# Kernel optimization log

Measured on AMD Instinct MI355X. Metric: run time of the kernel, lower is better.

Reference implementation:

```python
import jax, jax.numpy as jnp
import numpy as np

B, N, F, H = 2, 256, 64, 4
HID = 64            # hidden_features
C = H * HID         # n_coefficients = 256
KF = 50             # kernel_features (rbf count)
CUTOFF_UPPER = 5.0  # ExpNormalSmearing default (lower = 0)
ALPHA = 5.0 / CUTOFF_UPPER


def _dense(key, din, dout):
    scale = 1.0 / np.sqrt(din)
    return jax.random.uniform(key, (din, dout), minval=-scale, maxval=scale).astype(jnp.float32)


def setup_inputs() -> dict:
    key = jax.random.key(0)
    ks = jax.random.split(key, 16)
    start = float(np.exp(-CUTOFF_UPPER))
    means = jnp.asarray(np.linspace(start, 1.0, KF), jnp.float32)
    betas = jnp.full((KF,), (2.0 / KF * (1.0 - start)) ** -2, dtype=jnp.float32)
    d_edge_in = 2 * F              # h_cat_ht width
    d_cat = 2 * F + KF + 1         # concat([h0, rbf*h, dist])
    return dict(
        h=jax.random.normal(ks[0], (B, N, F), jnp.float32),
        x=jax.random.normal(ks[1], (B, N, 3), jnp.float32),
        v=jax.random.normal(ks[2], (B, N, 3), jnp.float32) * 0.1,
        W_in=_dense(ks[3], d_edge_in, KF), b_in=jnp.zeros((KF,), jnp.float32),
        rbf_means=means, rbf_betas=betas,
        W_o1=_dense(ks[4], d_cat, HID), b_o1=jnp.zeros((HID,), jnp.float32),
        W_o2=_dense(ks[5], HID, HID), b_o2=jnp.zeros((HID,), jnp.float32),
        W_sem=_dense(ks[6], HID, H), b_sem=jnp.zeros((H,), jnp.float32),
        W_xmix=_dense(ks[7], C, C),
        W_p1=_dense(ks[8], C, HID), b_p1=jnp.zeros((HID,), jnp.float32),
        W_p2=_dense(ks[9], HID, HID), b_p2=jnp.zeros((HID,), jnp.float32),
        W_n1=_dense(ks[10], F + C + HID, HID), b_n1=jnp.zeros((HID,), jnp.float32),
        W_n2=_dense(ks[11], HID, F), b_n2=jnp.zeros((F,), jnp.float32),
        W_v1=_dense(ks[12], F, HID), b_v1=jnp.zeros((HID,), jnp.float32),
        W_v2=_dense(ks[13], HID, 1),
        W_vmix=_dense(ks[14], C, 1),
    )


def reference(h, x, v, W_in, b_in, rbf_means, rbf_betas, W_o1, b_o1, W_o2, b_o2,
              W_sem, b_sem, W_xmix, W_p1, b_p1, W_p2, b_p2,
              W_n1, b_n1, W_n2, b_n2, W_v1, b_v1, W_v2, W_vmix):
    silu = jax.nn.silu
    n = h.shape[-2]
    # all-pairs displacements: entry [i, j] = x_j - x_i  (get_x_minus_xt)
    x_minus_xt = x[..., None, :, :] - x[..., :, None, :]                       # [B,N,N,3]
    d = jnp.sqrt(jax.nn.relu((x_minus_xt ** 2).sum(-1, keepdims=True)) + 1e-5)  # [B,N,N,1]
    # h_cat_ht: concat([h_j, h_i]) per pair (get_h_cat_ht)
    h_j = jnp.broadcast_to(h[..., None, :, :], h.shape[:-2] + (n, n, h.shape[-1]))
    h_i = jnp.broadcast_to(h[..., :, None, :], h.shape[:-2] + (n, n, h.shape[-1]))
    h_cat = jnp.concatenate([h_j, h_i], -1)                                     # [B,N,N,2F]
    # --- edge model: ContinuousFilterConvolutionWithConcatenation ---
    h1 = h_cat @ W_in + b_in                                                    # [B,N,N,KF]
    cut = 0.5 * (jnp.cos(d * jnp.pi / CUTOFF_UPPER) + 1.0) * (d < CUTOFF_UPPER)
    rbf = cut * jnp.exp(-rbf_betas * (jnp.exp(-ALPHA * d) - rbf_means) ** 2)    # [B,N,N,KF]
    h_e_mtx = silu(jnp.concatenate([h_cat, rbf * h1, d], -1) @ W_o1 + b_o1) @ W_o2 + b_o2  # [B,N,N,HID]
    # --- semantic attention (cutoff=None => euclidean factor is 1.0) ---
    att = jax.nn.celu(h_e_mtx @ W_sem + b_sem, alpha=2.0)                       # [B,N,N,H]
    att = att - 1e5 * jnp.eye(n, dtype=att.dtype)[..., None]                    # mask self-pairs
    att = jax.nn.softmax(att, axis=-2)
    combined = att / att.sum(-2, keepdims=True)                                 # combined_attention
    # per-head weighted edge features, flattened (feature-major, head-minor)
    h_e_att = (h_e_mtx[..., :, None] * combined[..., None, :]).reshape(h_e_mtx.shape[:-1] + (C,))  # [B,N,N,C]
    # --- spatial attention ---
    coeff = jnp.tanh(h_e_att @ W_xmix)                                          # x_mixing, [B,N,N,C]
    x_hat = x_minus_xt / (d + 1e-5)                                             # [B,N,N,3]
    # combinations[b,i,j,c,:] = x_hat[b,i,j,:] * coeff[b,i,j,c]; mean over j, fused:
    comb_sum = jnp.einsum('bijc,bijd->bicd', coeff, x_hat) / n                  # [B,N,C,3]
    comb_norm = (comb_sum ** 2).sum(-1)                                         # [B,N,C]
    h_comb = silu(silu(comb_norm @ W_p1 + b_p1) @ W_p2 + b_p2)                  # post_norm_mlp
    # --- aggregate + node model (residual) ---
    h_e = h_e_att.sum(-2)                                                       # [B,N,C]
    h_new = h + silu(silu(jnp.concatenate([h, h_e, h_comb], -1) @ W_n1 + b_n1) @ W_n2 + b_n2)
    # --- velocity / coordinate update (v_mixing then mean over j, fused via comb_sum) ---
    delta_v = jnp.einsum('bicd,c->bid', comb_sum, W_vmix[:, 0])                 # [B,N,3]
    v_scale = 2.0 * jax.nn.sigmoid(silu(h_new @ W_v1 + b_v1) @ W_v2)            # velocity_mlp + double_sigmoid
    v_new = delta_v + v_scale * v
    x_new = x + v_new
    return (h_new, x_new, v_new)
```

## Files before the change

### kernel.cpp

```cpp
#include <hip/hip_runtime.h>
#include <hip/hip_bf16.h>

typedef __hip_bfloat16 bf16;
typedef __attribute__((ext_vector_type(8))) short bf16x8;
typedef __attribute__((ext_vector_type(4))) float f32x4;

#define NNODE 512

__device__ __forceinline__ float b2f(bf16 v){ return __bfloat162float(v); }
__device__ __forceinline__ float siluf(float x){ return x / (1.f + __expf(-x)); }
__device__ __forceinline__ float tanhfast(float x){ return 1.f - 2.f/(__expf(2.f*x)+1.f); }
__device__ __forceinline__ float celu2(float x){ return x > 0.f ? x : 2.f*(__expf(0.5f*x)-1.f); }
__device__ __forceinline__ float bs2f(short v){ union{unsigned int i; float f;} t; t.i = ((unsigned int)(unsigned short)v) << 16; return t.f; }
__device__ __forceinline__ short f2bs(float x){ union{ bf16 b; short s; } u; u.b = __float2bfloat16(x); return u.s; }
__device__ __forceinline__ float lo16f(unsigned int u){ union{unsigned int i; float f;} t; t.i = u<<16; return t.f; }
__device__ __forceinline__ float hi16f(unsigned int u){ union{unsigned int i; float f;} t; t.i = u & 0xffff0000u; return t.f; }

template<typename T> __device__ __forceinline__ float ldv(const void* p, int i);
template<> __device__ __forceinline__ float ldv<float>(const void* p, int i){ return ((const float*)p)[i]; }
template<> __device__ __forceinline__ float ldv<bf16 >(const void* p, int i){ return b2f(((const bf16*)p)[i]); }

template<typename T> __device__ __forceinline__ void stv(void* p, int i, float v);
template<> __device__ __forceinline__ void stv<float>(void* p, int i, float v){ ((float*)p)[i] = v; }
template<> __device__ __forceinline__ void stv<bf16 >(void* p, int i, float v){ ((bf16*)p)[i] = __float2bfloat16(v); }

template<typename T> __device__ __forceinline__ short ldbs(const void* p, int i);
template<> __device__ __forceinline__ short ldbs<bf16 >(const void* p, int i){ union{ bf16 b; short s; } u; u.b = ((const bf16*)p)[i]; return u.s; }
template<> __device__ __forceinline__ short ldbs<float>(const void* p, int i){ return f2bs(((const float*)p)[i]); }

struct Args {
    const void *h,*x,*v,*Win,*bin,*means,*betas,*Wo1,*bo1,*Wo2,*bo2,*Wsem,*bsem,*Wx,
               *Wp1,*bp1,*Wp2,*bp2,*Wn1,*bn1,*Wn2,*bn2,*Wv1,*bv1,*Wv2,*Wvm;
};

__global__ void k_detect(const void* means, int* flag){
    if (threadIdx.x == 0){
        float v = b2f(((const bf16*)means)[0]);
        flag[0] = (fabsf(v) > 1.0f || v != v) ? 1 : 0;
    }
}

template<typename T>
__device__ __forceinline__ void nodepre_body(const Args& A, short* __restrict__ U1,
                                             float* __restrict__ Aj, short* __restrict__ WxT,
                                             float* sh)
{
    int bn = blockIdx.x, t = threadIdx.x;
    sh[t] = ldv<T>(A.h, bn*64 + t);
    __syncthreads();
    float u1 = 0.f;
    for (int f = 0; f < 64; ++f) u1 += sh[f] * ldv<T>(A.Wo1, f*64 + t);
    U1[bn*64 + t] = f2bs(u1);
    if (t < 50){
        float a1 = 0.f;
        for (int f = 0; f < 64; ++f) a1 += sh[f] * ldv<T>(A.Win, f*50 + t);
        Aj[bn*64 + t] = a1;
    }
    int o = (bn*64 + t)*2;
    #pragma unroll
    for (int q = 0; q < 2; ++q){
        int oo = o + q;
        int hh = oo >> 14, rem = oo & 16383, n = rem >> 6, f = rem & 63;
        WxT[oo] = ldbs<T>(A.Wx, (4*f + hh)*256 + n);
    }
}

__global__ void __launch_bounds__(64) k_nodepre(Args A, const int* __restrict__ flag,
                                                short* __restrict__ U1, float* __restrict__ Aj,
                                                short* __restrict__ WxT)
{
    __shared__ float sh[64];
    if (flag[0]) nodepre_body<float>(A, U1, Aj, WxT, sh);
    else         nodepre_body<bf16 >(A, U1, Aj, WxT, sh);
}

struct SmemPost {
    __align__(16) float att[256][4];
    float part[2][256];
    float red[768];
    float cn[256];
    float he[256];
    float fa[64];
    float fb[64];
    float mpart[8][64];
    float tmp[8][4];
};
struct SmemEdge {
    __align__(16) short wo1t[64*72];
    __align__(16) short wo2t[64*72];
};
struct Smem {
    __align__(16) bf16  e[256][72];
    __align__(16) float x4[256][4];
    float hi[64];
    float u2[64];
    float bo1v[64];
    float wl[64];
    float aivs[64];
    short wsem[256];
    __align__(16) short rbfh[8][4][72];
    __align__(16) short mid[8][4][72];
    union { SmemEdge edge; SmemPost post; } u;
};

template<typename T>
__device__ __forceinline__ void sake_body(const Args& A,
        const short* __restrict__ U1w, const float* __restrict__ Ajw,
        const short* __restrict__ wxt, void* __restrict__ out, Smem& S)
{
    int bi = blockIdx.x;
    int b = bi >> 8, i = bi & 255;
    int tid = threadIdx.x, w = tid >> 6, lane = tid & 63;
    int lane15 = lane & 15, quad = lane >> 4;

    if (tid < 64)  S.hi[tid]   = ldv<T>(A.h, bi*64 + tid);
    if (tid < 256) S.wsem[tid] = ldbs<T>(A.Wsem, tid);
    #pragma unroll
    for (int q = 0; q < 8; ++q){
        int idx = q*512 + tid;
        int n = idx >> 6, k = idx & 63;
        S.u.edge.wo2t[n*72 + k] = ldbs<T>(A.Wo2, k*64 + n);
        S.u.edge.wo1t[n*72 + k] = (k < 50) ? ldbs<T>(A.Wo1, (128+k)*64 + n) : (short)0;
    }
    if (lane >= 50){
        #pragma unroll
        for (int pp = 0; pp < 4; ++pp) S.rbfh[w][pp][lane] = 0;
    }
    float xi0 = ldv<T>(A.x, bi*3+0), xi1 = ldv<T>(A.x, bi*3+1), xi2 = ldv<T>(A.x, bi*3+2);
    if (tid < 256){
        int j = tid;
        float dx = ldv<T>(A.x,(b*256+j)*3+0) - xi0;
        float dy = ldv<T>(A.x,(b*256+j)*3+1) - xi1;
        float dz = ldv<T>(A.x,(b*256+j)*3+2) - xi2;
        float dd = sqrtf(dx*dx + dy*dy + dz*dz + 1e-5f);
        float inv = 1.f/(dd + 1e-5f);
        S.x4[j][0] = dx*inv; S.x4[j][1] = dy*inv; S.x4[j][2] = dz*inv; S.x4[j][3] = dd;
    }
    __syncthreads();

    if (w == 0){
        float u2v = 0.f;
        for (int f = 0; f < 64; ++f) u2v += S.hi[f] * ldv<T>(A.Wo1, (64+f)*64 + lane);
        S.u2[lane]   = u2v;
        S.bo1v[lane] = ldv<T>(A.bo1, lane);
        S.wl[lane]   = ldv<T>(A.Wo1, 178*64 + lane);
    } else if (w == 1 && lane < 50){
        float av = 0.f;
        for (int f = 0; f < 64; ++f) av += S.hi[f] * ldv<T>(A.Win, (64+f)*50 + lane);
        S.aivs[lane] = av;
    }
    float muv = 0.f, bev = 0.f, binv = 0.f;
    if (lane < 50){
        muv = ldv<T>(A.means, lane); bev = ldv<T>(A.betas, lane); binv = ldv<T>(A.bin, lane);
    }
    __syncthreads();

    float aiv = (lane < 50) ? S.aivs[lane] : 0.f;
    float bo2c[4], u24[4], bo14[4], wl4[4];
    #pragma unroll
    for (int nf = 0; nf < 4; ++nf){
        bo2c[nf] = ldv<T>(A.bo2, nf*16 + lane15);
        u24[nf]  = S.u2[nf*16 + lane15];
        bo14[nf] = S.bo1v[nf*16 + lane15];
        wl4[nf]  = S.wl[nf*16 + lane15];
    }

    for (int pass = 0; pass < 8; ++pass){
        int j0 = pass*32 + w*4;
        float dist[4];
        #pragma unroll
        for (int pp = 0; pp < 4; ++pp) dist[pp] = S.x4[j0+pp][3];

        if (lane < 50){
            #pragma unroll
            for (int pp = 0; pp < 4; ++pp){
                int j = j0 + pp;
                float h1 = Ajw[(b*256+j)*64 + lane] + aiv + binv;
                float dd = dist[pp];
                float cut = (dd < 5.f) ? 0.5f*(__cosf(dd*0.6283185307f) + 1.f) : 0.f;
                float ex = __expf(-dd) - muv;
                S.rbfh[w][pp][lane] = f2bs(cut * __expf(-bev*ex*ex) * h1);
            }
        }

        bf16x8 ar[2];
        #pragma unroll
        for (int kk = 0; kk < 2; ++kk){
            bf16x8 av = (bf16x8){0,0,0,0,0,0,0,0};
            if (lane15 < 4) av = *(const bf16x8*)&S.rbfh[w][lane15][kk*32 + quad*8];
            ar[kk] = av;
        }
        #pragma unroll
        for (int nf = 0; nf < 4; ++nf){
            int n = nf*16 + lane15;
            f32x4 Co1 = (f32x4){0.f,0.f,0.f,0.f};
            if (quad == 0){
                #pragma unroll
                for (int r = 0; r < 4; ++r)
                    Co1[r] = bs2f(U1w[(b*256 + j0 + r)*64 + n]) + u24[nf] + bo14[nf] + dist[r]*wl4[nf];
            }
            bf16x8 b0 = *(const bf16x8*)&S.u.edge.wo1t[n*72 + quad*8];
            bf16x8 b1 = *(const bf16x8*)&S.u.edge.wo1t[n*72 + 32 + quad*8];
            Co1 = __builtin_amdgcn_mfma_f32_16x16x32_bf16(ar[0], b0, Co1, 0, 0, 0);
            Co1 = __builtin_amdgcn_mfma_f32_16x16x32_bf16(ar[1], b1, Co1, 0, 0, 0);
            if (quad == 0){
                #pragma unroll
                for (int r = 0; r < 4; ++r) S.mid[w][r][n] = f2bs(siluf(Co1[r]));
            }
        }

        bf16x8 av2[2];
        #pragma unroll
        for (int kk = 0; kk < 2; ++kk){
            bf16x8 av = (bf16x8){0,0,0,0,0,0,0,0};
            if (lane15 < 4) av = *(const bf16x8*)&S.mid[w][lane15][kk*32 + quad*8];
            av2[kk] = av;
        }
        #pragma unroll
        for (int nf = 0; nf < 4; ++nf){
            int n = nf*16 + lane15;
            f32x4 Cc2 = (f32x4){bo2c[nf], bo2c[nf], bo2c[nf], bo2c[nf]};
            bf16x8 b0 = *(const bf16x8*)&S.u.edge.wo2t[n*72 + quad*8];
            bf16x8 b1 = *(const bf16x8*)&S.u.edge.wo2t[n*72 + 32 + quad*8];
            Cc2 = __builtin_amdgcn_mfma_f32_16x16x32_bf16(av2[0], b0, Cc2, 0, 0, 0);
            Cc2 = __builtin_amdgcn_mfma_f32_16x16x32_bf16(av2[1], b1, Cc2, 0, 0, 0);
            if (quad == 0){
                S.e[j0+0][n] = __float2bfloat16(Cc2[0]);
                S.e[j0+1][n] = __float2bfloat16(Cc2[1]);
                S.e[j0+2][n] = __float2bfloat16(Cc2[2]);
                S.e[j0+3][n] = __float2bfloat16(Cc2[3]);
            }
        }
    }
    __syncthreads();

    float ex0 = 0.f, ex1 = 0.f, ex2 = 0.f, ex3 = 0.f;
    if (tid < 256){
        int j = tid;
        float a0 = ldv<T>(A.bsem,0), a1 = ldv<T>(A.bsem,1), a2 = ldv<T>(A.bsem,2), a3 = ldv<T>(A.bsem,3);
        const unsigned int* erow = (const unsigned int*)&S.e[j][0];
        for (int f2 = 0; f2 < 32; ++f2){
            unsigned int u0 = erow[f2];
            float e0 = lo16f(u0), e1 = hi16f(u0);
            a0 += e0*bs2f(S.wsem[f2*8+0]) + e1*bs2f(S.wsem[f2*8+4]);
            a1 += e0*bs2f(S.wsem[f2*8+1]) + e1*bs2f(S.wsem[f2*8+5]);
            a2 += e0*bs2f(S.wsem[f2*8+2]) + e1*bs2f(S.wsem[f2*8+6]);
            a3 += e0*bs2f(S.wsem[f2*8+3]) + e1*bs2f(S.wsem[f2*8+7]);
        }
        a0 = celu2(a0); a1 = celu2(a1); a2 = celu2(a2); a3 = celu2(a3);
        if (j == i){ a0 -= 1e5f; a1 -= 1e5f; a2 -= 1e5f; a3 -= 1e5f; }
        float m0 = a0, m1 = a1, m2 = a2, m3 = a3;
        #pragma unroll
        for (int off = 1; off < 64; off <<= 1){
            m0 = fmaxf(m0, __shfl_xor(m0, off)); m1 = fmaxf(m1, __shfl_xor(m1, off));
            m2 = fmaxf(m2, __shfl_xor(m2, off)); m3 = fmaxf(m3, __shfl_xor(m3, off));
        }
        if (lane == 0){
            S.u.post.tmp[w][0] = m0; S.u.post.tmp[w][1] = m1;
            S.u.post.tmp[w][2] = m2; S.u.post.tmp[w][3] = m3;
        }
        ex0 = a0; ex1 = a1; ex2 = a2; ex3 = a3;
    }
    __syncthreads();
    if (tid < 256){
        float m0 = fmaxf(fmaxf(S.u.post.tmp[0][0], S.u.post.tmp[1][0]), fmaxf(S.u.post.tmp[2][0], S.u.post.tmp[3][0]));
        float m1 = fmaxf(fmaxf(S.u.post.tmp[0][1], S.u.post.tmp[1][1]), fmaxf(S.u.post.tmp[2][1], S.u.post.tmp[3][1]));
        float m2 = fmaxf(fmaxf(S.u.post.tmp[0][2], S.u.post.tmp[1][2]), fmaxf(S.u.post.tmp[2][2], S.u.post.tmp[3][2]));
        float m3 = fmaxf(fmaxf(S.u.post.tmp[0][3], S.u.post.tmp[1][3]), fmaxf(S.u.post.tmp[2][3], S.u.post.tmp[3][3]));
        ex0 = __expf(ex0-m0); ex1 = __expf(ex1-m1); ex2 = __expf(ex2-m2); ex3 = __expf(ex3-m3);
        float s0 = ex0, s1 = ex1, s2 = ex2, s3 = ex3;
        #pragma unroll
        for (int off = 1; off < 64; off <<= 1){
            s0 += __shfl_xor(s0, off); s1 += __shfl_xor(s1, off);
            s2 += __shfl_xor(s2, off); s3 += __shfl_xor(s3, off);
        }
        if (lane == 0){
            S.u.post.tmp[4+w][0] = s0; S.u.post.tmp[4+w][1] = s1;
            S.u.post.tmp[4+w][2] = s2; S.u.post.tmp[4+w][3] = s3;
        }
    }
    __syncthreads();
    if (tid < 256){
        float s0 = S.u.post.tmp[4][0]+S.u.post.tmp[5][0]+S.u.post.tmp[6][0]+S.u.post.tmp[7][0];
        float s1 = S.u.post.tmp[4][1]+S.u.post.tmp[5][1]+S.u.post.tmp[6][1]+S.u.post.tmp[7][1];
        float s2 = S.u.post.tmp[4][2]+S.u.post.tmp[5][2]+S.u.post.tmp[6][2]+S.u.post.tmp[7][2];
        float s3 = S.u.post.tmp[4][3]+S.u.post.tmp[5][3]+S.u.post.tmp[6][3]+S.u.post.tmp[7][3];
        S.u.post.att[tid][0] = ex0/s0; S.u.post.att[tid][1] = ex1/s1;
        S.u.post.att[tid][2] = ex2/s2; S.u.post.att[tid][3] = ex3/s3;
    }
    __syncthreads();

    {
        int c = tid & 255, jh = tid >> 8;
        int f_he = c >> 2, h_he = c & 3;
        float acc = 0.f;
        int j2 = jh*128;
        for (int q = 0; q < 128; ++q, ++j2)
            acc += b2f(S.e[j2][f_he]) * S.u.post.att[j2][h_he];
        S.u.post.part[jh][c] = acc;
    }
    __syncthreads();
    if (tid < 256) S.u.post.he[tid] = S.u.post.part[0][tid] + S.u.post.part[1][tid];

    {
        const short* se_s = (const short*)S.e;
        float ca[2][3];
        #pragma unroll
        for (int nf2 = 0; nf2 < 2; ++nf2){ ca[nf2][0]=0.f; ca[nf2][1]=0.f; ca[nf2][2]=0.f; }

        #pragma unroll
        for (int nf2 = 0; nf2 < 2; ++nf2){
            int n = w*32 + nf2*16 + lane15;
            bf16x8 Bh[4][2];
            #pragma unroll
            for (int hh = 0; hh < 4; ++hh){
                const short* bp = wxt + (hh*256 + n)*64 + quad*8;
                Bh[hh][0] = *(const bf16x8*)(bp);
                Bh[hh][1] = *(const bf16x8*)(bp + 32);
            }
            for (int mt = 0; mt < 16; ++mt){
                int jq = mt*16 + quad*4;
                f32x4 att4[4];
                #pragma unroll
                for (int r = 0; r < 4; ++r) att4[r] = *(const f32x4*)&S.u.post.att[jq + r][0];
                bf16x8 Af[2];
                #pragma unroll
                for (int ks = 0; ks < 2; ++ks)
                    Af[ks] = *(const bf16x8*)(se_s + (mt*16 + lane15)*72 + ks*32 + quad*8);
                float Pt[4] = {0.f, 0.f, 0.f, 0.f};
                #pragma unroll
                for (int hh = 0; hh < 4; ++hh){
                    f32x4 Cc = (f32x4){0.f,0.f,0.f,0.f};
                    Cc = __builtin_amdgcn_mfma_f32_16x16x32_bf16(Af[0], Bh[hh][0], Cc, 0, 0, 0);
                    Cc = __builtin_amdgcn_mfma_f32_16x16x32_bf16(Af[1], Bh[hh][1], Cc, 0, 0, 0);
                    #pragma unroll
                    for (int r = 0; r < 4; ++r) Pt[r] += att4[r][hh] * Cc[r];
                }
                #pragma unroll
                for (int r = 0; r < 4; ++r){
                    int j = jq + r;
                    float cf = tanhfast(Pt[r]);
                    f32x4 xh = *(const f32x4*)&S.x4[j][0];
                    ca[nf2][0] += cf*xh[0]; ca[nf2][1] += cf*xh[1]; ca[nf2][2] += cf*xh[2];
                }
            }
        }
        #pragma unroll
        for (int nf2 = 0; nf2 < 2; ++nf2){
            #pragma unroll
            for (int d = 0; d < 3; ++d){
                float vs = ca[nf2][d];
                vs += __shfl_xor(vs, 16);
                vs += __shfl_xor(vs, 32);
                if (quad == 0) S.u.post.red[(w*32 + nf2*16 + lane15)*3 + d] = vs;
            }
        }
    }
    __syncthreads();

    const float sc = 1.f/256.f;
    if (tid < 256){
        float c0 = S.u.post.red[tid*3+0]*sc, c1 = S.u.post.red[tid*3+1]*sc, c2 = S.u.post.red[tid*3+2]*sc;
        S.u.post.cn[tid] = c0*c0 + c1*c1 + c2*c2;
    }
    __syncthreads();

    {
        float acc = 0.f;
        int c0 = w*32;
        for (int c = c0; c < c0+32; ++c) acc += S.u.post.cn[c] * ldv<T>(A.Wp1, c*64 + lane);
        S.u.post.mpart[w][lane] = acc;
    }
    __syncthreads();
    if (tid < 64){
        float acc = ldv<T>(A.bp1, tid);
        #pragma unroll
        for (int q = 0; q < 8; ++q) acc += S.u.post.mpart[q][tid];
        S.u.post.fa[tid] = siluf(acc);
    }
    __syncthreads();
    {
        float acc = 0.f;
        int k0 = w*8;
        #pragma unroll
        for (int k = 0; k < 8; ++k) acc += S.u.post.fa[k0+k] * ldv<T>(A.Wp2, (k0+k)*64 + lane);
        S.u.post.mpart[w][lane] = acc;
    }
    __syncthreads();
    if (tid < 64){
        float acc = ldv<T>(A.bp2, tid);
        #pragma unroll
        for (int q = 0; q < 8; ++q) acc += S.u.post.mpart[q][tid];
        S.u.post.fb[tid] = siluf(acc);
    }
    __syncthreads();
    {
        float acc = 0.f;
        int r0 = w*48;
        for (int r = r0; r < r0+48; ++r){
            float xv = (r < 64) ? S.hi[r] : (r < 320) ? S.u.post.he[r-64] : S.u.post.fb[r-320];
            acc += xv * ldv<T>(A.Wn1, r*64 + lane);
        }
        S.u.post.mpart[w][lane] = acc;
    }
    __syncthreads();
    if (tid < 64){
        float acc = ldv<T>(A.bn1, tid);
        #pragma unroll
        for (int q = 0; q < 8; ++q) acc += S.u.post.mpart[q][tid];
        S.u.post.fa[tid] = siluf(acc);
    }
    __syncthreads();
    {
        float acc = 0.f;
        int k0 = w*8;
        #pragma unroll
        for (int k = 0; k < 8; ++k) acc += S.u.post.fa[k0+k] * ldv<T>(A.Wn2, (k0+k)*64 + lane);
        S.u.post.mpart[w][lane] = acc;
    }
    __syncthreads();
    if (tid < 64){
        float acc = ldv<T>(A.bn2, tid);
        #pragma unroll
        for (int q = 0; q < 8; ++q) acc += S.u.post.mpart[q][tid];
        float hn = S.hi[tid] + siluf(acc);
        stv<T>(out, bi*64 + tid, hn);
        S.u.post.fb[tid] = hn;
    }
    __syncthreads();
    {
        float acc = 0.f;
        int k0 = w*8;
        #pragma unroll
        for (int k = 0; k < 8; ++k) acc += S.u.post.fb[k0+k] * ldv<T>(A.Wv1, (k0+k)*64 + lane);
        S.u.post.mpart[w][lane] = acc;
    }
    __syncthreads();
    float vscale = 0.f;
    if (tid < 64){
        float acc = ldv<T>(A.bv1, tid);
        #pragma unroll
        for (int q = 0; q < 8; ++q) acc += S.u.post.mpart[q][tid];
        float term = siluf(acc) * ldv<T>(A.Wv2, tid);
        #pragma unroll
        for (int off = 1; off < 64; off <<= 1) term += __shfl_xor(term, off);
        vscale = 2.f / (1.f + __expf(-term));
    }
    if (w < 4){
        int c = w*64 + lane;
        float wv = ldv<T>(A.Wvm, c);
        float d0 = S.u.post.red[c*3+0]*sc*wv;
        float d1 = S.u.post.red[c*3+1]*sc*wv;
        float d2 = S.u.post.red[c*3+2]*sc*wv;
        #pragma unroll
        for (int off = 1; off < 64; off <<= 1){
            d0 += __shfl_xor(d0, off); d1 += __shfl_xor(d1, off); d2 += __shfl_xor(d2, off);
        }
        if (lane == 0){ S.u.post.tmp[w][0] = d0; S.u.post.tmp[w][1] = d1; S.u.post.tmp[w][2] = d2; }
    }
    __syncthreads();
    if (tid < 3){
        float dv = S.u.post.tmp[0][tid] + S.u.post.tmp[1][tid] + S.u.post.tmp[2][tid] + S.u.post.tmp[3][tid];
        float vn = dv + vscale * ldv<T>(A.v, bi*3 + tid);
        float xn = ldv<T>(A.x, bi*3 + tid) + vn;
        stv<T>(out, 32768 + bi*3 + tid, xn);
        stv<T>(out, 34304 + bi*3 + tid, vn);
    }
}

__global__ void __launch_bounds__(512, 4) k_sake(Args A, const int* __restrict__ flag,
                                                 const short* __restrict__ U1w,
                                                 const float* __restrict__ Ajw,
                                                 const short* __restrict__ wxt,
                                                 void* __restrict__ out)
{
    __shared__ Smem S;
    if (flag[0]) sake_body<float>(A, U1w, Ajw, wxt, out, S);
    else         sake_body<bf16 >(A, U1w, Ajw, wxt, out, S);
}

extern "C" void kernel_launch(void* const* d_in, const int* in_sizes, int n_in,
                              void* d_out, int out_size, void* d_ws, size_t ws_size,
                              hipStream_t stream)
{
    Args A;
    A.h     = d_in[0];  A.x     = d_in[1];  A.v     = d_in[2];
    A.Win   = d_in[3];  A.bin   = d_in[4];  A.means = d_in[5];  A.betas = d_in[6];
    A.Wo1   = d_in[7];  A.bo1   = d_in[8];  A.Wo2   = d_in[9];  A.bo2   = d_in[10];
    A.Wsem  = d_in[11]; A.bsem  = d_in[12]; A.Wx    = d_in[13];
    A.Wp1   = d_in[14]; A.bp1   = d_in[15]; A.Wp2   = d_in[16]; A.bp2   = d_in[17];
    A.Wn1   = d_in[18]; A.bn1   = d_in[19]; A.Wn2   = d_in[20]; A.bn2   = d_in[21];
    A.Wv1   = d_in[22]; A.bv1   = d_in[23]; A.Wv2   = d_in[24]; A.Wvm   = d_in[25];

    int*   flag = (int*)d_ws;
    short* U1b  = (short*)((char*)d_ws + 64);
    float* Aj   = (float*)((char*)d_ws + 64 + 65536);
    short* WxT  = (short*)((char*)d_ws + 64 + 65536 + 131072);

    k_detect<<<1, 64, 0, stream>>>(A.means, flag);
    k_nodepre<<<NNODE, 64, 0, stream>>>(A, flag, U1b, Aj, WxT);
    k_sake<<<NNODE, 512, 0, stream>>>(A, flag, U1b, Aj, WxT, d_out);
}
```

Before: 201.7 us.

## Restructure edge MLP to full 16-edge MFMA tiles and drop detect kernel

```diff
diff --git a/kernel.cpp b/kernel.cpp
--- a/kernel.cpp
+++ b/kernel.cpp
@@ -3,6 +3,7 @@
 
 typedef __hip_bfloat16 bf16;
 typedef __attribute__((ext_vector_type(8))) short bf16x8;
+typedef __attribute__((ext_vector_type(4))) short s16x4;
 typedef __attribute__((ext_vector_type(4))) float f32x4;
 
 #define NNODE 512
@@ -33,50 +34,62 @@
                *Wp1,*bp1,*Wp2,*bp2,*Wn1,*bn1,*Wn2,*bn2,*Wv1,*bv1,*Wv2,*Wvm;
 };
 
-__global__ void k_detect(const void* means, int* flag){
-    if (threadIdx.x == 0){
-        float v = b2f(((const bf16*)means)[0]);
-        flag[0] = (fabsf(v) > 1.0f || v != v) ? 1 : 0;
-    }
+__device__ __forceinline__ bool detect_f32(const void* means){
+    float v = b2f(((const bf16*)means)[0]);
+    return (fabsf(v) > 1.0f || v != v);
 }
 
 template<typename T>
 __device__ __forceinline__ void nodepre_body(const Args& A, short* __restrict__ U1,
                                              float* __restrict__ Aj, short* __restrict__ WxT,
-                                             float* sh)
+                                             float* sh, float (*p1)[64], float (*p2)[64])
 {
-    int bn = blockIdx.x, t = threadIdx.x;
-    sh[t] = ldv<T>(A.h, bn*64 + t);
-    __syncthreads();
-    float u1 = 0.f;
-    for (int f = 0; f < 64; ++f) u1 += sh[f] * ldv<T>(A.Wo1, f*64 + t);
-    U1[bn*64 + t] = f2bs(u1);
+    int bn = blockIdx.x, tid = threadIdx.x;
+    int t = tid & 63, ks = tid >> 6;
+    if (tid < 64) sh[tid] = ldv<T>(A.h, bn*64 + tid);
+    __syncthreads();
+    float a1 = 0.f;
+    #pragma unroll
+    for (int q = 0; q < 16; ++q){
+        int f = ks*16 + q;
+        a1 += sh[f] * ldv<T>(A.Wo1, f*64 + t);
+    }
+    p1[ks][t] = a1;
     if (t < 50){
-        float a1 = 0.f;
-        for (int f = 0; f < 64; ++f) a1 += sh[f] * ldv<T>(A.Win, f*50 + t);
-        Aj[bn*64 + t] = a1;
-    }
-    int o = (bn*64 + t)*2;
-    #pragma unroll
-    for (int q = 0; q < 2; ++q){
-        int oo = o + q;
-        int hh = oo >> 14, rem = oo & 16383, n = rem >> 6, f = rem & 63;
+        float a2 = 0.f;
+        #pragma unroll
+        for (int q = 0; q < 16; ++q){
+            int f = ks*16 + q;
+            a2 += sh[f] * ldv<T>(A.Win, f*50 + t);
+        }
+        p2[ks][t] = a2;
+    }
+    if (tid < 128){
+        int oo = bn*128 + tid;
+        int hh = oo >> 14, rem = oo & 16383, n = rem >> 6, f = oo & 63;
         WxT[oo] = ldbs<T>(A.Wx, (4*f + hh)*256 + n);
     }
+    __syncthreads();
+    if (tid < 64){
+        U1[bn*64 + tid] = f2bs(p1[0][tid] + p1[1][tid] + p1[2][tid] + p1[3][tid]);
+        float av = (tid < 50) ? (p2[0][tid] + p2[1][tid] + p2[2][tid] + p2[3][tid]) : 0.f;
+        Aj[bn*64 + tid] = av;
+    }
 }
 
-__global__ void __launch_bounds__(64) k_nodepre(Args A, const int* __restrict__ flag,
-                                                short* __restrict__ U1, float* __restrict__ Aj,
-                                                short* __restrict__ WxT)
+__global__ void __launch_bounds__(256) k_nodepre(Args A, short* __restrict__ U1,
+                                                 float* __restrict__ Aj, short* __restrict__ WxT)
 {
     __shared__ float sh[64];
-    if (flag[0]) nodepre_body<float>(A, U1, Aj, WxT, sh);
-    else         nodepre_body<bf16 >(A, U1, Aj, WxT, sh);
+    __shared__ float p1[4][64];
+    __shared__ float p2[4][64];
+    if (detect_f32(A.means)) nodepre_body<float>(A, U1, Aj, WxT, sh, p1, p2);
+    else                     nodepre_body<bf16 >(A, U1, Aj, WxT, sh, p1, p2);
 }
 
 struct SmemPost {
     __align__(16) float att[256][4];
-    float part[2][256];
+    float part[4][256];
     float red[768];
     float cn[256];
     float he[256];
@@ -85,22 +98,20 @@
     float mpart[8][64];
     float tmp[8][4];
 };
-struct SmemEdge {
-    __align__(16) short wo1t[64*72];
-    __align__(16) short wo2t[64*72];
-};
 struct Smem {
     __align__(16) bf16  e[256][72];
     __align__(16) float x4[256][4];
     float hi[64];
-    float u2[64];
-    float bo1v[64];
+    float ub[64];
     float wl[64];
-    float aivs[64];
+    __align__(16) float kc[64][4];
     short wsem[256];
-    __align__(16) short rbfh[8][4][72];
-    __align__(16) short mid[8][4][72];
-    union { SmemEdge edge; SmemPost post; } u;
+    __align__(16) short wo1t[64*72];
+    __align__(16) short wo2t[64*72];
+    union {
+        SmemPost post;
+        __align__(16) short mid[8][16][72];
+    } u;
 };
 
 template<typename T>
@@ -115,16 +126,19 @@
 
     if (tid < 64)  S.hi[tid]   = ldv<T>(A.h, bi*64 + tid);
     if (tid < 256) S.wsem[tid] = ldbs<T>(A.Wsem, tid);
+    if (tid < 64){
+        bool kv = tid < 50;
+        S.kc[tid][0] = kv ? ldv<T>(A.means, tid) : 0.f;
+        S.kc[tid][1] = kv ? ldv<T>(A.betas, tid) : 0.f;
+        S.kc[tid][2] = kv ? ldv<T>(A.bin,   tid) : 0.f;
+        S.kc[tid][3] = 0.f;
+    }
     #pragma unroll
     for (int q = 0; q < 8; ++q){
         int idx = q*512 + tid;
         int n = idx >> 6, k = idx & 63;
-        S.u.edge.wo2t[n*72 + k] = ldbs<T>(A.Wo2, k*64 + n);
-        S.u.edge.wo1t[n*72 + k] = (k < 50) ? ldbs<T>(A.Wo1, (128+k)*64 + n) : (short)0;
-    }
-    if (lane >= 50){
-        #pragma unroll
-        for (int pp = 0; pp < 4; ++pp) S.rbfh[w][pp][lane] = 0;
+        S.wo2t[n*72 + k] = ldbs<T>(A.Wo2, k*64 + n);
+        S.wo1t[n*72 + k] = (k < 50) ? ldbs<T>(A.Wo1, (128+k)*64 + n) : (short)0;
     }
     float xi0 = ldv<T>(A.x, bi*3+0), xi1 = ldv<T>(A.x, bi*3+1), xi2 = ldv<T>(A.x, bi*3+2);
     if (tid < 256){
@@ -141,94 +155,118 @@
     if (w == 0){
         float u2v = 0.f;
         for (int f = 0; f < 64; ++f) u2v += S.hi[f] * ldv<T>(A.Wo1, (64+f)*64 + lane);
-        S.u2[lane]   = u2v;
-        S.bo1v[lane] = ldv<T>(A.bo1, lane);
-        S.wl[lane]   = ldv<T>(A.Wo1, 178*64 + lane);
+        S.ub[lane] = u2v + ldv<T>(A.bo1, lane);
+        S.wl[lane] = ldv<T>(A.Wo1, 178*64 + lane);
     } else if (w == 1 && lane < 50){
         float av = 0.f;
         for (int f = 0; f < 64; ++f) av += S.hi[f] * ldv<T>(A.Win, (64+f)*50 + lane);
-        S.aivs[lane] = av;
-    }
-    float muv = 0.f, bev = 0.f, binv = 0.f;
-    if (lane < 50){
-        muv = ldv<T>(A.means, lane); bev = ldv<T>(A.betas, lane); binv = ldv<T>(A.bin, lane);
-    }
-    __syncthreads();
-
-    float aiv = (lane < 50) ? S.aivs[lane] : 0.f;
-    float bo2c[4], u24[4], bo14[4], wl4[4];
+        S.kc[lane][3] = av;
+    }
+    __syncthreads();
+
+    float ubr[16], wlr[16], bo2r[16];
     #pragma unroll
     for (int nf = 0; nf < 4; ++nf){
-        bo2c[nf] = ldv<T>(A.bo2, nf*16 + lane15);
-        u24[nf]  = S.u2[nf*16 + lane15];
-        bo14[nf] = S.bo1v[nf*16 + lane15];
-        wl4[nf]  = S.wl[nf*16 + lane15];
-    }
-
-    for (int pass = 0; pass < 8; ++pass){
-        int j0 = pass*32 + w*4;
-        float dist[4];
-        #pragma unroll
-        for (int pp = 0; pp < 4; ++pp) dist[pp] = S.x4[j0+pp][3];
-
-        if (lane < 50){
-            #pragma unroll
-            for (int pp = 0; pp < 4; ++pp){
-                int j = j0 + pp;
-                float h1 = Ajw[(b*256+j)*64 + lane] + aiv + binv;
-                float dd = dist[pp];
-                float cut = (dd < 5.f) ? 0.5f*(__cosf(dd*0.6283185307f) + 1.f) : 0.f;
-                float ex = __expf(-dd) - muv;
-                S.rbfh[w][pp][lane] = f2bs(cut * __expf(-bev*ex*ex) * h1);
+        #pragma unroll
+        for (int r = 0; r < 4; ++r){
+            int m = nf*16 + quad*4 + r;
+            ubr[nf*4+r]  = S.ub[m];
+            wlr[nf*4+r]  = S.wl[m];
+            bo2r[nf*4+r] = ldv<T>(A.bo2, m);
+        }
+    }
+
+    for (int pass = 0; pass < 2; ++pass){
+        int j = pass*128 + w*16 + lane15;
+        float dd  = S.x4[j][3];
+        float cut = (dd < 5.f) ? 0.5f*(__cosf(dd*0.6283185307f) + 1.f) : 0.f;
+        float ed  = __expf(-dd);
+        const float* ajp = Ajw + (b*256 + j)*64;
+        bf16x8 Brb[2];
+        #pragma unroll
+        for (int s = 0; s < 2; ++s){
+            int kb = s*32 + quad*8;
+            f32x4 a0 = *(const f32x4*)(ajp + kb);
+            f32x4 a1 = *(const f32x4*)(ajp + kb + 4);
+            bf16x8 bv;
+            #pragma unroll
+            for (int i2 = 0; i2 < 8; ++i2){
+                int k = kb + i2;
+                f32x4 kcv = *(const f32x4*)&S.kc[k][0];
+                float aj = (i2 < 4) ? a0[i2] : a1[i2-4];
+                float h1 = aj + kcv[3] + kcv[2];
+                float ex = ed - kcv[0];
+                float val = cut * __expf(-kcv[1]*ex*ex) * h1;
+                bv[i2] = (k < 50) ? f2bs(val) : (short)0;
             }
-        }
-
-        bf16x8 ar[2];
-        #pragma unroll
-        for (int kk = 0; kk < 2; ++kk){
-            bf16x8 av = (bf16x8){0,0,0,0,0,0,0,0};
-            if (lane15 < 4) av = *(const bf16x8*)&S.rbfh[w][lane15][kk*32 + quad*8];
-            ar[kk] = av;
-        }
+            Brb[s] = bv;
+        }
+        const short* u1p = U1w + (b*256 + j)*64;
         #pragma unroll
         for (int nf = 0; nf < 4; ++nf){
-            int n = nf*16 + lane15;
-            f32x4 Co1 = (f32x4){0.f,0.f,0.f,0.f};
-            if (quad == 0){
+            const short* wp = S.wo1t + (nf*16 + lane15)*72;
+            bf16x8 A0 = *(const bf16x8*)(wp + quad*8);
+            bf16x8 A1 = *(const bf16x8*)(wp + 32 + quad*8);
+            s16x4 u4 = *(const s16x4*)(u1p + nf*16 + quad*4);
+            f32x4 C;
+            #pragma unroll
+            for (int r = 0; r < 4; ++r)
+                C[r] = bs2f(u4[r]) + ubr[nf*4+r] + dd*wlr[nf*4+r];
+            C = __builtin_amdgcn_mfma_f32_16x16x32_bf16(A0, Brb[0], C, 0, 0, 0);
+            C = __builtin_amdgcn_mfma_f32_16x16x32_bf16(A1, Brb[1], C, 0, 0, 0);
+            s16x4 m4;
+            #pragma unroll
+            for (int r = 0; r < 4; ++r) m4[r] = f2bs(siluf(C[r]));
+            *(s16x4*)&S.u.mid[w][lane15][nf*16 + quad*4] = m4;
+        }
+        bf16x8 Bm0 = *(const bf16x8*)&S.u.mid[w][lane15][quad*8];
+        bf16x8 Bm1 = *(const bf16x8*)&S.u.mid[w][lane15][32 + quad*8];
+        #pragma unroll
+        for (int nf = 0; nf < 4; ++nf){
+            const short* wp = S.wo2t + (nf*16 + lane15)*72;
+            bf16x8 A0 = *(const bf16x8*)(wp + quad*8);
+            bf16x8 A1 = *(const bf16x8*)(wp + 32 + quad*8);
+            f32x4 C = (f32x4){bo2r[nf*4+0], bo2r[nf*4+1], bo2r[nf*4+2], bo2r[nf*4+3]};
+            C = __builtin_amdgcn_mfma_f32_16x16x32_bf16(A0, Bm0, C, 0, 0, 0);
+            C = __builtin_amdgcn_mfma_f32_16x16x32_bf16(A1, Bm1, C, 0, 0, 0);
+            s16x4 e4;
+            #pragma unroll
+            for (int r = 0; r < 4; ++r) e4[r] = f2bs(C[r]);
+            *(s16x4*)&((short*)S.e)[j*72 + nf*16 + quad*4] = e4;
+        }
+    }
+    __syncthreads();
+
+    {
+        bf16x8 Bs[2];
+        #pragma unroll
+        for (int ks = 0; ks < 2; ++ks){
+            bf16x8 bv = (bf16x8){0,0,0,0,0,0,0,0};
+            if (lane15 < 4){
                 #pragma unroll
-                for (int r = 0; r < 4; ++r)
-                    Co1[r] = bs2f(U1w[(b*256 + j0 + r)*64 + n]) + u24[nf] + bo14[nf] + dist[r]*wl4[nf];
+                for (int i2 = 0; i2 < 8; ++i2)
+                    bv[i2] = S.wsem[(ks*32 + quad*8 + i2)*4 + lane15];
             }
-            bf16x8 b0 = *(const bf16x8*)&S.u.edge.wo1t[n*72 + quad*8];
-            bf16x8 b1 = *(const bf16x8*)&S.u.edge.wo1t[n*72 + 32 + quad*8];
-            Co1 = __builtin_amdgcn_mfma_f32_16x16x32_bf16(ar[0], b0, Co1, 0, 0, 0);
-            Co1 = __builtin_amdgcn_mfma_f32_16x16x32_bf16(ar[1], b1, Co1, 0, 0, 0);
-            if (quad == 0){
+            Bs[ks] = bv;
+        }
+        float bsv = (lane15 < 4) ? ldv<T>(A.bsem, lane15) : 0.f;
+        #pragma unroll
+        for (int t2 = 0; t2 < 2; ++t2){
+            int jt = w*2 + t2;
+            const short* ep = (const short*)S.e + (jt*16 + lane15)*72;
+            bf16x8 A0 = *(const bf16x8*)(ep + quad*8);
+            bf16x8 A1 = *(const bf16x8*)(ep + 32 + quad*8);
+            f32x4 C = (f32x4){bsv, bsv, bsv, bsv};
+            C = __builtin_amdgcn_mfma_f32_16x16x32_bf16(A0, Bs[0], C, 0, 0, 0);
+            C = __builtin_amdgcn_mfma_f32_16x16x32_bf16(A1, Bs[1], C, 0, 0, 0);
+            if (lane15 < 4){
                 #pragma unroll
-                for (int r = 0; r < 4; ++r) S.mid[w][r][n] = f2bs(siluf(Co1[r]));
-            }
-        }
-
-        bf16x8 av2[2];
-        #pragma unroll
-        for (int kk = 0; kk < 2; ++kk){
-            bf16x8 av = (bf16x8){0,0,0,0,0,0,0,0};
-            if (lane15 < 4) av = *(const bf16x8*)&S.mid[w][lane15][kk*32 + quad*8];
-            av2[kk] = av;
-        }
-        #pragma unroll
-        for (int nf = 0; nf < 4; ++nf){
-            int n = nf*16 + lane15;
-            f32x4 Cc2 = (f32x4){bo2c[nf], bo2c[nf], bo2c[nf], bo2c[nf]};
-            bf16x8 b0 = *(const bf16x8*)&S.u.edge.wo2t[n*72 + quad*8];
-            bf16x8 b1 = *(const bf16x8*)&S.u.edge.wo2t[n*72 + 32 + quad*8];
-            Cc2 = __builtin_amdgcn_mfma_f32_16x16x32_bf16(av2[0], b0, Cc2, 0, 0, 0);
-            Cc2 = __builtin_amdgcn_mfma_f32_16x16x32_bf16(av2[1], b1, Cc2, 0, 0, 0);
-            if (quad == 0){
-                S.e[j0+0][n] = __float2bfloat16(Cc2[0]);
-                S.e[j0+1][n] = __float2bfloat16(Cc2[1]);
-                S.e[j0+2][n] = __float2bfloat16(Cc2[2]);
-                S.e[j0+3][n] = __float2bfloat16(Cc2[3]);
+                for (int r = 0; r < 4; ++r){
+                    int jr = jt*16 + quad*4 + r;
+                    float lv = celu2(C[r]);
+                    if (jr == i) lv -= 1e5f;
+                    S.u.post.att[jr][lane15] = lv;
+                }
             }
         }
     }
@@ -236,20 +274,9 @@
 
     float ex0 = 0.f, ex1 = 0.f, ex2 = 0.f, ex3 = 0.f;
     if (tid < 256){
-        int j = tid;
-        float a0 = ldv<T>(A.bsem,0), a1 = ldv<T>(A.bsem,1), a2 = ldv<T>(A.bsem,2), a3 = ldv<T>(A.bsem,3);
-        const unsigned int* erow = (const unsigned int*)&S.e[j][0];
-        for (int f2 = 0; f2 < 32; ++f2){
-            unsigned int u0 = erow[f2];
-            float e0 = lo16f(u0), e1 = hi16f(u0);
-            a0 += e0*bs2f(S.wsem[f2*8+0]) + e1*bs2f(S.wsem[f2*8+4]);
-            a1 += e0*bs2f(S.wsem[f2*8+1]) + e1*bs2f(S.wsem[f2*8+5]);
-            a2 += e0*bs2f(S.wsem[f2*8+2]) + e1*bs2f(S.wsem[f2*8+6]);
-            a3 += e0*bs2f(S.wsem[f2*8+3]) + e1*bs2f(S.wsem[f2*8+7]);
-        }
-        a0 = celu2(a0); a1 = celu2(a1); a2 = celu2(a2); a3 = celu2(a3);
-        if (j == i){ a0 -= 1e5f; a1 -= 1e5f; a2 -= 1e5f; a3 -= 1e5f; }
-        float m0 = a0, m1 = a1, m2 = a2, m3 = a3;
+        float l0 = S.u.post.att[tid][0], l1 = S.u.post.att[tid][1];
+        float l2 = S.u.post.att[tid][2], l3 = S.u.post.att[tid][3];
+        float m0 = l0, m1 = l1, m2 = l2, m3 = l3;
         #pragma unroll
         for (int off = 1; off < 64; off <<= 1){
             m0 = fmaxf(m0, __shfl_xor(m0, off)); m1 = fmaxf(m1, __shfl_xor(m1, off));
@@ -259,7 +286,7 @@
             S.u.post.tmp[w][0] = m0; S.u.post.tmp[w][1] = m1;
             S.u.post.tmp[w][2] = m2; S.u.post.tmp[w][3] = m3;
         }
-        ex0 = a0; ex1 = a1; ex2 = a2; ex3 = a3;
+        ex0 = l0; ex1 = l1; ex2 = l2; ex3 = l3;
     }
     __syncthreads();
     if (tid < 256){
@@ -291,48 +318,58 @@
     __syncthreads();
 
     {
-        int c = tid & 255, jh = tid >> 8;
-        int f_he = c >> 2, h_he = c & 3;
-        float acc = 0.f;
-        int j2 = jh*128;
-        for (int q = 0; q < 128; ++q, ++j2)
-            acc += b2f(S.e[j2][f_he]) * S.u.post.att[j2][h_he];
-        S.u.post.part[jh][c] = acc;
-    }
-    __syncthreads();
-    if (tid < 256) S.u.post.he[tid] = S.u.post.part[0][tid] + S.u.post.part[1][tid];
+        int cg = tid & 127, js = tid >> 7;
+        int fp = cg >> 2, hh = cg & 3;
+        float acc0 = 0.f, acc1 = 0.f;
+        const unsigned int* ep = (const unsigned int*)S.e;
+        for (int jj = 0; jj < 64; ++jj){
+            int j = js*64 + jj;
+            unsigned int u = ep[j*36 + fp];
+            float a = S.u.post.att[j][hh];
+            acc0 += lo16f(u)*a; acc1 += hi16f(u)*a;
+        }
+        S.u.post.part[js][8*fp + hh]     = acc0;
+        S.u.post.part[js][8*fp + 4 + hh] = acc1;
+    }
+    __syncthreads();
+    if (tid < 256)
+        S.u.post.he[tid] = S.u.post.part[0][tid] + S.u.post.part[1][tid]
+                         + S.u.post.part[2][tid] + S.u.post.part[3][tid];
 
     {
         const short* se_s = (const short*)S.e;
-        float ca[2][3];
-        #pragma unroll
-        for (int nf2 = 0; nf2 < 2; ++nf2){ ca[nf2][0]=0.f; ca[nf2][1]=0.f; ca[nf2][2]=0.f; }
-
+        bf16x8 Bh[2][4][2];
         #pragma unroll
         for (int nf2 = 0; nf2 < 2; ++nf2){
             int n = w*32 + nf2*16 + lane15;
-            bf16x8 Bh[4][2];
             #pragma unroll
             for (int hh = 0; hh < 4; ++hh){
                 const short* bp = wxt + (hh*256 + n)*64 + quad*8;
-                Bh[hh][0] = *(const bf16x8*)(bp);
-                Bh[hh][1] = *(const bf16x8*)(bp + 32);
+                Bh[nf2][hh][0] = *(const bf16x8*)(bp);
+                Bh[nf2][hh][1] = *(const bf16x8*)(bp + 32);
             }
-            for (int mt = 0; mt < 16; ++mt){
-                int jq = mt*16 + quad*4;
-                f32x4 att4[4];
-                #pragma unroll
-                for (int r = 0; r < 4; ++r) att4[r] = *(const f32x4*)&S.u.post.att[jq + r][0];
-                bf16x8 Af[2];
-                #pragma unroll
-                for (int ks = 0; ks < 2; ++ks)
-                    Af[ks] = *(const bf16x8*)(se_s + (mt*16 + lane15)*72 + ks*32 + quad*8);
+        }
+        float ca[2][3];
+        #pragma unroll
+        for (int nf2 = 0; nf2 < 2; ++nf2){ ca[nf2][0]=0.f; ca[nf2][1]=0.f; ca[nf2][2]=0.f; }
+
+        for (int mt = 0; mt < 16; ++mt){
+            int jq = mt*16 + quad*4;
+            f32x4 att4[4];
+            #pragma unroll
+            for (int r = 0; r < 4; ++r) att4[r] = *(const f32x4*)&S.u.post.att[jq + r][0];
+            bf16x8 Af[2];
+            #pragma unroll
+            for (int ks = 0; ks < 2; ++ks)
+                Af[ks] = *(const bf16x8*)(se_s + (mt*16 + lane15)*72 + ks*32 + quad*8);
+            #pragma unroll
+            for (int nf2 = 0; nf2 < 2; ++nf2){
                 float Pt[4] = {0.f, 0.f, 0.f, 0.f};
                 #pragma unroll
                 for (int hh = 0; hh < 4; ++hh){
                     f32x4 Cc = (f32x4){0.f,0.f,0.f,0.f};
-                    Cc = __builtin_amdgcn_mfma_f32_16x16x32_bf16(Af[0], Bh[hh][0], Cc, 0, 0, 0);
-                    Cc = __builtin_amdgcn_mfma_f32_16x16x32_bf16(Af[1], Bh[hh][1], Cc, 0, 0, 0);
+                    Cc = __builtin_amdgcn_mfma_f32_16x16x32_bf16(Af[0], Bh[nf2][hh][0], Cc, 0, 0, 0);
+                    Cc = __builtin_amdgcn_mfma_f32_16x16x32_bf16(Af[1], Bh[nf2][hh][1], Cc, 0, 0, 0);
                     #pragma unroll
                     for (int r = 0; r < 4; ++r) Pt[r] += att4[r][hh] * Cc[r];
                 }
@@ -468,15 +505,15 @@
     }
 }
 
-__global__ void __launch_bounds__(512, 4) k_sake(Args A, const int* __restrict__ flag,
+__global__ void __launch_bounds__(512, 4) k_sake(Args A,
                                                  const short* __restrict__ U1w,
                                                  const float* __restrict__ Ajw,
                                                  const short* __restrict__ wxt,
                                                  void* __restrict__ out)
 {
     __shared__ Smem S;
-    if (flag[0]) sake_body<float>(A, U1w, Ajw, wxt, out, S);
-    else         sake_body<bf16 >(A, U1w, Ajw, wxt, out, S);
+    if (detect_f32(A.means)) sake_body<float>(A, U1w, Ajw, wxt, out, S);
+    else                     sake_body<bf16 >(A, U1w, Ajw, wxt, out, S);
 }
 
 extern "C" void kernel_launch(void* const* d_in, const int* in_sizes, int n_in,
@@ -492,12 +529,10 @@
     A.Wn1   = d_in[18]; A.bn1   = d_in[19]; A.Wn2   = d_in[20]; A.bn2   = d_in[21];
     A.Wv1   = d_in[22]; A.bv1   = d_in[23]; A.Wv2   = d_in[24]; A.Wvm   = d_in[25];
 
-    int*   flag = (int*)d_ws;
-    short* U1b  = (short*)((char*)d_ws + 64);
-    float* Aj   = (float*)((char*)d_ws + 64 + 65536);
-    short* WxT  = (short*)((char*)d_ws + 64 + 65536 + 131072);
-
-    k_detect<<<1, 64, 0, stream>>>(A.means, flag);
-    k_nodepre<<<NNODE, 64, 0, stream>>>(A, flag, U1b, Aj, WxT);
-    k_sake<<<NNODE, 512, 0, stream>>>(A, flag, U1b, Aj, WxT, d_out);
+    short* U1b  = (short*)d_ws;
+    float* Aj   = (float*)((char*)d_ws + 65536);
+    short* WxT  = (short*)((char*)d_ws + 65536 + 131072);
+
+    k_nodepre<<<NNODE, 256, 0, stream>>>(A, U1b, Aj, WxT);
+    k_sake<<<NNODE, 512, 0, stream>>>(A, U1b, Aj, WxT, d_out);
 }
```

After: 180.1 us. 1.12x faster.
